# Optimization experiments

Measured on AMD Instinct MI355X. Metric: run time of the kernel, lower is better.

## Reference

```python
import jax, jax.numpy as jnp
import numpy as np

N, E, FIN, NH, FOUT = 50000, 800000, 128, 4, 16


def setup_inputs() -> dict:
    key = jax.random.key(0)
    ks = jax.random.split(key, 6)
    x = jax.random.normal(ks[0], (N, FIN), dtype=jnp.float32)
    edge_index = jax.random.randint(ks[1], (2, E), 0, N, dtype=jnp.int64)
    w_proj = jax.random.normal(ks[2], (NH * FOUT, FIN), dtype=jnp.float32) * 0.05
    a_src = jax.random.normal(ks[3], (NH, FOUT), dtype=jnp.float32) * 0.1
    a_trg = jax.random.normal(ks[4], (NH, FOUT), dtype=jnp.float32) * 0.1
    w_skip = jax.random.normal(ks[5], (NH * FOUT, FIN), dtype=jnp.float32) * 0.05
    return {"x": x, "edge_index": edge_index, "w_proj": w_proj,
            "a_src": a_src, "a_trg": a_trg, "w_skip": w_skip}


def reference(x, edge_index, w_proj, a_src, a_trg, w_skip):
    # Dropout is identity in eval mode.
    src, trg = edge_index[0], edge_index[1]
    # Project: [N, NH, FOUT]
    proj = (x @ w_proj.T).reshape(N, NH, FOUT)
    # Per-node attention logits: [N, NH]
    s_src = jnp.einsum('nhf,hf->nh', proj, a_src)
    s_trg = jnp.einsum('nhf,hf->nh', proj, a_trg)
    # Lift to edges and score: [E, NH]
    scores = jax.nn.leaky_relu(s_src[src] + s_trg[trg], negative_slope=0.2)
    # Global-max-shifted exp (matches original, which subtracts the global max)
    exp_scores = jnp.exp(scores - jnp.max(scores))
    # Segment-wise softmax denominator over target nodes
    denom = jax.ops.segment_sum(exp_scores, trg, num_segments=N)  # [N, NH]
    attn = exp_scores / (denom[trg] + 1e-16)                      # [E, NH]
    # Weighted aggregation of lifted source features: [N, NH, FOUT]
    weighted = proj[src] * attn[:, :, None]
    agg = jax.ops.segment_sum(weighted, trg, num_segments=N)
    # Skip projection (FOUT != FIN branch) and concat over heads
    out = agg + (x @ w_skip.T).reshape(N, NH, FOUT)
    out = out.reshape(N, NH * FOUT)
    return jax.nn.elu(out)
```

## Files before the change

### kernel.cpp

```cpp
#include <hip/hip_runtime.h>
#include <cstddef>

#define N_NODES 50000
#define N_EDGES 800000
#define FIN     128
#define NH      4
#define FOUT    16
#define COUT    64
#define STRIPS  (N_NODES / 16)
#define PAIRS   ((STRIPS + 1) / 2)
#define SCAN_BLOCKS ((N_NODES + 255) / 256)
#define NB      128
#define CHUNK   (N_EDGES / NB)
#define HW4     (N_NODES / 4)
#define HBYTES  (HW4 * 4)
#define NQ      4
#define BPQ     (NB / NQ)
#define PBLK    ((HW4 + 255) / 256)
#define E4      (N_EDGES / 4)
#define E4B     ((E4 + 255) / 256)

typedef __bf16 bf16x8 __attribute__((ext_vector_type(8)));
typedef float  f32x4  __attribute__((ext_vector_type(4)));

__global__ __launch_bounds__(256) void k1_mfma(
    const float* __restrict__ x, const __bf16* __restrict__ wb,
    const float* __restrict__ asrc, const float* __restrict__ atrg,
    __bf16* __restrict__ projb, float* __restrict__ ssrc, float* __restrict__ strg,
    float* __restrict__ outv)
{
    const int lane = threadIdx.x & 63;
    const int wid  = blockIdx.x * 4 + (threadIdx.x >> 6);
    const int pair = wid >> 1;
    const int half = wid & 1;
    if (pair >= PAIRS) return;
    const int r = lane & 15;
    const int g = lane >> 4;
    const int row0 = pair * 32;

    bf16x8 bfr[4][4];
    #pragma unroll
    for (int j = 0; j < 4; ++j) {
        const __bf16* wrow = wb + (size_t)(half * 64 + j * 16 + r) * FIN;
        #pragma unroll
        for (int kk = 0; kk < 4; ++kk)
            bfr[j][kk] = *reinterpret_cast<const bf16x8*>(wrow + kk * 32 + g * 8);
    }

    const int rowA0 = row0 + r;
    int rowA1 = row0 + 16 + r;
    if (rowA1 >= N_NODES) rowA1 = N_NODES - 1;
    const float* xr0 = x + (size_t)rowA0 * FIN + g * 8;
    const float* xr1 = x + (size_t)rowA1 * FIN + g * 8;
    bf16x8 af0[4], af1[4];
    #pragma unroll
    for (int kk = 0; kk < 4; ++kk) {
        float4 u0 = *reinterpret_cast<const float4*>(xr0 + kk * 32);
        float4 u1 = *reinterpret_cast<const float4*>(xr0 + kk * 32 + 4);
        float4 v0 = *reinterpret_cast<const float4*>(xr1 + kk * 32);
        float4 v1 = *reinterpret_cast<const float4*>(xr1 + kk * 32 + 4);
        bf16x8 a, b;
        a[0] = (__bf16)u0.x; a[1] = (__bf16)u0.y;
        a[2] = (__bf16)u0.z; a[3] = (__bf16)u0.w;
        a[4] = (__bf16)u1.x; a[5] = (__bf16)u1.y;
        a[6] = (__bf16)u1.z; a[7] = (__bf16)u1.w;
        b[0] = (__bf16)v0.x; b[1] = (__bf16)v0.y;
        b[2] = (__bf16)v0.z; b[3] = (__bf16)v0.w;
        b[4] = (__bf16)v1.x; b[5] = (__bf16)v1.y;
        b[6] = (__bf16)v1.z; b[7] = (__bf16)v1.w;
        af0[kk] = a; af1[kk] = b;
    }

    f32x4 acc0[4] = {{0.f,0.f,0.f,0.f},{0.f,0.f,0.f,0.f},
                     {0.f,0.f,0.f,0.f},{0.f,0.f,0.f,0.f}};
    f32x4 acc1[4] = {{0.f,0.f,0.f,0.f},{0.f,0.f,0.f,0.f},
                     {0.f,0.f,0.f,0.f},{0.f,0.f,0.f,0.f}};
    #pragma unroll
    for (int kk = 0; kk < 4; ++kk)
        #pragma unroll
        for (int j = 0; j < 4; ++j) {
            acc0[j] = __builtin_amdgcn_mfma_f32_16x16x32_bf16(
                          af0[kk], bfr[j][kk], acc0[j], 0, 0, 0);
            acc1[j] = __builtin_amdgcn_mfma_f32_16x16x32_bf16(
                          af1[kk], bfr[j][kk], acc1[j], 0, 0, 0);
        }

    if (!half) {
        #pragma unroll
        for (int j = 0; j < 4; ++j)
            #pragma unroll
            for (int q = 0; q < 4; ++q) {
                int n0 = row0 + g * 4 + q;
                int n1 = n0 + 16;
                projb[(size_t)n0 * COUT + j * 16 + r] = (__bf16)acc0[j][q];
                if (n1 < N_NODES)
                    projb[(size_t)n1 * COUT + j * 16 + r] = (__bf16)acc1[j][q];
            }
        #pragma unroll
        for (int j = 0; j < 4; ++j) {
            const float as = asrc[j * 16 + r];
            const float at = atrg[j * 16 + r];
            #pragma unroll
            for (int q = 0; q < 4; ++q) {
                float ts0 = acc0[j][q] * as, tt0 = acc0[j][q] * at;
                float ts1 = acc1[j][q] * as, tt1 = acc1[j][q] * at;
                ts0 += __shfl_xor(ts0, 1); ts0 += __shfl_xor(ts0, 2);
                ts0 += __shfl_xor(ts0, 4); ts0 += __shfl_xor(ts0, 8);
                tt0 += __shfl_xor(tt0, 1); tt0 += __shfl_xor(tt0, 2);
                tt0 += __shfl_xor(tt0, 4); tt0 += __shfl_xor(tt0, 8);
                ts1 += __shfl_xor(ts1, 1); ts1 += __shfl_xor(ts1, 2);
                ts1 += __shfl_xor(ts1, 4); ts1 += __shfl_xor(ts1, 8);
                tt1 += __shfl_xor(tt1, 1); tt1 += __shfl_xor(tt1, 2);
                tt1 += __shfl_xor(tt1, 4); tt1 += __shfl_xor(tt1, 8);
                if (r == 0) {
                    int n0 = row0 + g * 4 + q;
                    int n1 = n0 + 16;
                    ssrc[(size_t)n0 * NH + j] = ts0;
                    strg[(size_t)n0 * NH + j] = tt0;
                    if (n1 < N_NODES) {
                        ssrc[(size_t)n1 * NH + j] = ts1;
                        strg[(size_t)n1 * NH + j] = tt1;
                    }
                }
            }
        }
    } else {
        #pragma unroll
        for (int j = 0; j < 4; ++j)
            #pragma unroll
            for (int q = 0; q < 4; ++q) {
                int n0 = row0 + g * 4 + q;
                int n1 = n0 + 16;
                outv[(size_t)n0 * COUT + j * 16 + r] = acc0[j][q];
                if (n1 < N_NODES)
                    outv[(size_t)n1 * COUT + j * 16 + r] = acc1[j][q];
            }
    }
}

__global__ __launch_bounds__(1024) void k_hist(
    const int* __restrict__ ei, unsigned* __restrict__ histG,
    unsigned char* __restrict__ rank,
    const float* __restrict__ wproj, const float* __restrict__ wskip,
    __bf16* __restrict__ wb, int* __restrict__ scounter)
{
    if (blockIdx.x == NB) {
        const int tid = threadIdx.x;
        if (tid == 0) *scounter = 0;
        for (int gid = tid; gid < (128 * FIN) / 4; gid += 1024) {
            int row = gid >> 5;
            float4 v = (row < 64)
                ? reinterpret_cast<const float4*>(wproj)[gid]
                : reinterpret_cast<const float4*>(wskip)[gid - 2048];
            __bf16* o = wb + (size_t)gid * 4;
            o[0] = (__bf16)v.x; o[1] = (__bf16)v.y;
            o[2] = (__bf16)v.z; o[3] = (__bf16)v.w;
        }
        return;
    }
    extern __shared__ unsigned h[];
    const int t = threadIdx.x;
    for (int i = t; i < HW4; i += 1024) h[i] = 0;
    __syncthreads();
    const int base = blockIdx.x * CHUNK;
    for (int i = t; i < CHUNK; i += 1024) {
        int tg = ei[N_EDGES + base + i];
        int sh = (tg & 3) * 8;
        unsigned old = atomicAdd(&h[tg >> 2], 1u << sh);
        rank[base + i] = (unsigned char)((old >> sh) & 0xffu);
    }
    __syncthreads();
    unsigned* out = histG + (size_t)blockIdx.x * HW4;
    for (int i = t; i < HW4; i += 1024) out[i] = h[i];
}

__global__ __launch_bounds__(256) void k_colscanA(
    const unsigned* __restrict__ histG, unsigned* __restrict__ offG,
    unsigned* __restrict__ partial)
{
    int p = blockIdx.x * 256 + threadIdx.x;
    if (p >= HW4) return;
    int q = blockIdx.y;
    unsigned run = 0;
    #pragma unroll 4
    for (int b = q * BPQ; b < (q + 1) * BPQ; ++b) {
        unsigned v = histG[(size_t)b * HW4 + p];
        offG[(size_t)b * HW4 + p] = run;
        run += v;
    }
    partial[(size_t)q * HW4 + p] = run;
}

__global__ __launch_bounds__(256) void k_scanfuse(
    const unsigned* __restrict__ partial, unsigned* __restrict__ baseQ,
    int* __restrict__ deg, int* __restrict__ tmpExc,
    int* __restrict__ bsum, int* __restrict__ bOff,
    int* __restrict__ scounter)
{
    __shared__ int sm[256];
    __shared__ int isLast;
    const int t = threadIdx.x;
    if (t < 64) {
        int p = blockIdx.x * 64 + t;
        if (p < HW4) {
            unsigned s = 0;
            #pragma unroll
            for (int q = 0; q < NQ; ++q) {
                baseQ[(size_t)q * HW4 + p] = s;
                s += partial[(size_t)q * HW4 + p];
            }
            int4 d4 = make_int4((int)(s & 0xffu), (int)((s >> 8) & 0xffu),
                                (int)((s >> 16) & 0xffu), (int)(s >> 24));
            reinterpret_cast<int4*>(deg)[p] = d4;
            sm[4 * t + 0] = d4.x; sm[4 * t + 1] = d4.y;
            sm[4 * t + 2] = d4.z; sm[4 * t + 3] = d4.w;
        } else {
            sm[4 * t + 0] = 0; sm[4 * t + 1] = 0;
            sm[4 * t + 2] = 0; sm[4 * t + 3] = 0;
        }
    }
    __syncthreads();
    int v = sm[t];
    #pragma unroll
    for (int off = 1; off < 256; off <<= 1) {
        int x = (t >= off) ? sm[t - off] : 0;
        __syncthreads();
        sm[t] += x;
        __syncthreads();
    }
    int i = blockIdx.x * 256 + t;
    if (i < N_NODES) tmpExc[i] = sm[t] - v;
    if (t == 255) atomicExch(&bsum[blockIdx.x], sm[t]);
    __syncthreads();
    if (t == 0) {
        __threadfence();
        int old = atomicAdd(scounter, 1);
        isLast = (old == SCAN_BLOCKS - 1) ? 1 : 0;
    }
    __syncthreads();
    if (isLast) {
        int bv = (t < SCAN_BLOCKS) ? atomicAdd(&bsum[t], 0) : 0;
        sm[t] = bv;
        __syncthreads();
        #pragma unroll
        for (int off = 1; off < 256; off <<= 1) {
            int x = (t >= off) ? sm[t - off] : 0;
            __syncthreads();
            sm[t] += x;
            __syncthreads();
        }
        if (t < SCAN_BLOCKS) bOff[t] = sm[t] - bv;
    }
}

__global__ __launch_bounds__(256) void k_scatter(
    const int* __restrict__ ei, const unsigned char* __restrict__ rank,
    const unsigned* __restrict__ offG, const unsigned* __restrict__ baseQ,
    const int* __restrict__ tmpExc, const int* __restrict__ bOff,
    int* __restrict__ srcs)
{
    int e4 = blockIdx.x * 256 + threadIdx.x;
    if (e4 >= E4) return;
    int4 s4 = reinterpret_cast<const int4*>(ei)[e4];
    int4 t4 = reinterpret_cast<const int4*>(ei + N_EDGES)[e4];
    uchar4 r4 = reinterpret_cast<const uchar4*>(rank)[e4];
    const int e0 = e4 * 4;
    int ss[4] = {s4.x, s4.y, s4.z, s4.w};
    int tt[4] = {t4.x, t4.y, t4.z, t4.w};
    int rr[4] = {r4.x, r4.y, r4.z, r4.w};
    #pragma unroll
    for (int u = 0; u < 4; ++u) {
        int tg = tt[u];
        int b  = (e0 + u) / CHUNK;
        int sh = (tg & 3) * 8;
        unsigned cw = offG[(size_t)b * HW4 + (tg >> 2)]
                    + baseQ[(size_t)(b / BPQ) * HW4 + (tg >> 2)];
        int cross = (int)((cw >> sh) & 0xffu);
        int slot  = tmpExc[tg] + bOff[tg >> 8] + cross + rr[u];
        srcs[slot] = ss[u];
    }
}

__global__ __launch_bounds__(256) void k3_gather(
    const int* __restrict__ tmpExc, const int* __restrict__ bOff,
    const int* __restrict__ deg, const int* __restrict__ srcs,
    const float* __restrict__ ssrc, const float* __restrict__ strg,
    const __bf16* __restrict__ projb, float* __restrict__ outv)
{
    const int lane = threadIdx.x & 63;
    const int node = __builtin_amdgcn_readfirstlane(blockIdx.x * 4 + (threadIdx.x >> 6));
    if (node >= N_NODES) return;
    const int h = lane >> 4;
    const int begin = tmpExc[node] + bOff[node >> 8];
    const int dg    = deg[node];
    const float st  = strg[(size_t)node * NH + h];
    const float skip = outv[(size_t)node * COUT + lane];

    float acc = 0.f, dsum = 0.f;
    int i = 0;
    for (; i + 8 <= dg; i += 8) {
        int s[8]; float a[8], p[8];
        #pragma unroll
        for (int u = 0; u < 8; ++u) s[u] = srcs[begin + i + u];
        #pragma unroll
        for (int u = 0; u < 8; ++u) a[u] = ssrc[(size_t)s[u] * NH + h];
        #pragma unroll
        for (int u = 0; u < 8; ++u) p[u] = (float)projb[(size_t)s[u] * COUT + lane];
        #pragma unroll
        for (int u = 0; u < 8; ++u) {
            float z = a[u] + st;
            z = (z >= 0.f) ? z : 0.2f * z;
            float ez = __expf(z);
            dsum += ez;
            acc += ez * p[u];
        }
    }
    for (; i + 4 <= dg; i += 4) {
        int s[4]; float a[4], p[4];
        #pragma unroll
        for (int u = 0; u < 4; ++u) s[u] = srcs[begin + i + u];
        #pragma unroll
        for (int u = 0; u < 4; ++u) a[u] = ssrc[(size_t)s[u] * NH + h];
        #pragma unroll
        for (int u = 0; u < 4; ++u) p[u] = (float)projb[(size_t)s[u] * COUT + lane];
        #pragma unroll
        for (int u = 0; u < 4; ++u) {
            float z = a[u] + st;
            z = (z >= 0.f) ? z : 0.2f * z;
            float ez = __expf(z);
            dsum += ez;
            acc += ez * p[u];
        }
    }
    for (; i < dg; ++i) {
        int s = srcs[begin + i];
        float z = ssrc[(size_t)s * NH + h] + st;
        z = (z >= 0.f) ? z : 0.2f * z;
        float ez = __expf(z);
        float p  = (float)projb[(size_t)s * COUT + lane];
        dsum += ez;
        acc += ez * p;
    }
    float o = acc / (dsum + 1e-16f) + skip;
    o = (o > 0.f) ? o : expm1f(o);
    outv[(size_t)node * COUT + lane] = o;
}

extern "C" void kernel_launch(void* const* d_in, const int* in_sizes, int n_in,
                              void* d_out, int out_size, void* d_ws, size_t ws_size,
                              hipStream_t stream)
{
    const float* x     = (const float*)d_in[0];
    const int*   ei    = (const int*)  d_in[1];
    const float* wproj = (const float*)d_in[2];
    const float* asrc  = (const float*)d_in[3];
    const float* atrg  = (const float*)d_in[4];
    const float* wskip = (const float*)d_in[5];
    float* outv = (float*)d_out;

    __bf16* projb = (__bf16*)d_ws;
    float* base  = (float*)d_ws;
    float* ssrc  = base + (size_t)N_NODES * COUT;
    float* strg  = ssrc + (size_t)N_NODES * NH;
    int* deg     = (int*)(strg + (size_t)N_NODES * NH);
    int* tmpExc  = deg    + N_NODES;
    int* bsum    = tmpExc + N_NODES;
    int* bOff    = bsum   + 256;
    int* srcs    = bOff   + 256;
    unsigned* histG   = (unsigned*)(srcs + N_EDGES);
    unsigned* offG    = histG + (size_t)NB * HW4;
    unsigned* partial = offG  + (size_t)NB * HW4;
    unsigned* baseQ   = partial + (size_t)NQ * HW4;
    unsigned char* rank = (unsigned char*)(baseQ + (size_t)NQ * HW4);
    __bf16* wb   = (__bf16*)(rank + N_EDGES);
    int* scounter = (int*)(wb + 128 * FIN);

    k_hist<<<NB + 1, 1024, HBYTES, stream>>>(ei, histG, rank,
                                             wproj, wskip, wb, scounter);

    int k1_blocks = (PAIRS * 2 + 3) / 4;
    k1_mfma<<<k1_blocks, 256, 0, stream>>>(x, wb, asrc, atrg,
                                           projb, ssrc, strg, outv);

    k_colscanA<<<dim3(PBLK, NQ), 256, 0, stream>>>(histG, offG, partial);

    k_scanfuse<<<SCAN_BLOCKS, 256, 0, stream>>>(partial, baseQ, deg,
                                                tmpExc, bsum, bOff, scounter);

    k_scatter<<<E4B, 256, 0, stream>>>(ei, rank, offG, baseQ,
                                       tmpExc, bOff, srcs);

    int k3_blocks = (N_NODES + 3) / 4;
    k3_gather<<<k3_blocks, 256, 0, stream>>>(tmpExc, bOff, deg, srcs,
                                             ssrc, strg, projb, outv);
}
```

Baseline: 95.02 us.

## Split histogram blocks by node range and fuse column scan into CSR scan

The histogram kernel now runs two blocks per edge chunk, each covering half of the packed node range, which halves shared memory per block so more blocks can be resident. Each block still reads every target in its chunk and discards those outside its half. The two-pass column scan and scan-fuse kernels are merged into one kernel in which four threads per packed word scan the quarters and combine them through shared memory, removing one launch and the partial buffer. The cost is that edge reads in the histogram are doubled.

```diff
diff --git a/kernel.cpp b/kernel.cpp
--- a/kernel.cpp
+++ b/kernel.cpp
@@ -13,10 +13,10 @@
 #define NB      128
 #define CHUNK   (N_EDGES / NB)
 #define HW4     (N_NODES / 4)
-#define HBYTES  (HW4 * 4)
+#define HALFW   (HW4 / 2)
+#define HBYTES2 (HALFW * 4)
 #define NQ      4
 #define BPQ     (NB / NQ)
-#define PBLK    ((HW4 + 255) / 256)
 #define E4      (N_EDGES / 4)
 #define E4B     ((E4 + 255) / 256)
 
@@ -144,7 +144,7 @@
     const float* __restrict__ wproj, const float* __restrict__ wskip,
     __bf16* __restrict__ wb, int* __restrict__ scounter)
 {
-    if (blockIdx.x == NB) {
+    if (blockIdx.x == NB * 2) {
         const int tid = threadIdx.x;
         if (tid == 0) *scounter = 0;
         for (int gid = tid; gid < (128 * FIN) / 4; gid += 1024) {
@@ -159,66 +159,67 @@
         return;
     }
     extern __shared__ unsigned h[];
+    const int chunk = blockIdx.x >> 1;
+    const int vhalf = blockIdx.x & 1;
     const int t = threadIdx.x;
-    for (int i = t; i < HW4; i += 1024) h[i] = 0;
-    __syncthreads();
-    const int base = blockIdx.x * CHUNK;
+    for (int i = t; i < HALFW; i += 1024) h[i] = 0;
+    __syncthreads();
+    const int base = chunk * CHUNK;
+    const int plo  = vhalf * HALFW;
     for (int i = t; i < CHUNK; i += 1024) {
         int tg = ei[N_EDGES + base + i];
-        int sh = (tg & 3) * 8;
-        unsigned old = atomicAdd(&h[tg >> 2], 1u << sh);
-        rank[base + i] = (unsigned char)((old >> sh) & 0xffu);
-    }
-    __syncthreads();
-    unsigned* out = histG + (size_t)blockIdx.x * HW4;
-    for (int i = t; i < HW4; i += 1024) out[i] = h[i];
-}
-
-__global__ __launch_bounds__(256) void k_colscanA(
+        int p  = (tg >> 2) - plo;
+        if ((unsigned)p < (unsigned)HALFW) {
+            int sh = (tg & 3) * 8;
+            unsigned old = atomicAdd(&h[p], 1u << sh);
+            rank[base + i] = (unsigned char)((old >> sh) & 0xffu);
+        }
+    }
+    __syncthreads();
+    unsigned* out = histG + (size_t)chunk * HW4 + plo;
+    for (int i = t; i < HALFW; i += 1024) out[i] = h[i];
+}
+
+__global__ __launch_bounds__(256) void k_csr_scan(
     const unsigned* __restrict__ histG, unsigned* __restrict__ offG,
-    unsigned* __restrict__ partial)
-{
-    int p = blockIdx.x * 256 + threadIdx.x;
-    if (p >= HW4) return;
-    int q = blockIdx.y;
-    unsigned run = 0;
-    #pragma unroll 4
-    for (int b = q * BPQ; b < (q + 1) * BPQ; ++b) {
-        unsigned v = histG[(size_t)b * HW4 + p];
-        offG[(size_t)b * HW4 + p] = run;
-        run += v;
-    }
-    partial[(size_t)q * HW4 + p] = run;
-}
-
-__global__ __launch_bounds__(256) void k_scanfuse(
-    const unsigned* __restrict__ partial, unsigned* __restrict__ baseQ,
+    unsigned* __restrict__ baseQ,
     int* __restrict__ deg, int* __restrict__ tmpExc,
     int* __restrict__ bsum, int* __restrict__ bOff,
     int* __restrict__ scounter)
 {
+    __shared__ unsigned part[64][NQ];
     __shared__ int sm[256];
     __shared__ int isLast;
-    const int t = threadIdx.x;
-    if (t < 64) {
-        int p = blockIdx.x * 64 + t;
-        if (p < HW4) {
-            unsigned s = 0;
-            #pragma unroll
-            for (int q = 0; q < NQ; ++q) {
-                baseQ[(size_t)q * HW4 + p] = s;
-                s += partial[(size_t)q * HW4 + p];
-            }
-            int4 d4 = make_int4((int)(s & 0xffu), (int)((s >> 8) & 0xffu),
-                                (int)((s >> 16) & 0xffu), (int)(s >> 24));
-            reinterpret_cast<int4*>(deg)[p] = d4;
-            sm[4 * t + 0] = d4.x; sm[4 * t + 1] = d4.y;
-            sm[4 * t + 2] = d4.z; sm[4 * t + 3] = d4.w;
-        } else {
-            sm[4 * t + 0] = 0; sm[4 * t + 1] = 0;
-            sm[4 * t + 2] = 0; sm[4 * t + 3] = 0;
-        }
-    }
+    const int t  = threadIdx.x;
+    const int pl = t >> 2;
+    const int q  = t & 3;
+    const int p  = blockIdx.x * 64 + pl;
+    const bool valid = (p < HW4);
+
+    unsigned run = 0;
+    if (valid) {
+        #pragma unroll 4
+        for (int b = q * BPQ; b < (q + 1) * BPQ; ++b) {
+            unsigned v = histG[(size_t)b * HW4 + p];
+            offG[(size_t)b * HW4 + p] = run;
+            run += v;
+        }
+    }
+    part[pl][q] = run;
+    __syncthreads();
+
+    unsigned p0 = part[pl][0], p1 = part[pl][1],
+             p2 = part[pl][2], p3 = part[pl][3];
+    unsigned pre = (q > 0 ? p0 : 0u) + (q > 1 ? p1 : 0u) + (q > 2 ? p2 : 0u);
+    unsigned total = p0 + p1 + p2 + p3;
+    if (valid) {
+        baseQ[(size_t)q * HW4 + p] = pre;
+        if (q == 0)
+            reinterpret_cast<int4*>(deg)[p] =
+                make_int4((int)(total & 0xffu), (int)((total >> 8) & 0xffu),
+                          (int)((total >> 16) & 0xffu), (int)(total >> 24));
+    }
+    sm[t] = valid ? (int)((total >> (q * 8)) & 0xffu) : 0;
     __syncthreads();
     int v = sm[t];
     #pragma unroll
@@ -369,22 +370,19 @@
     int* srcs    = bOff   + 256;
     unsigned* histG   = (unsigned*)(srcs + N_EDGES);
     unsigned* offG    = histG + (size_t)NB * HW4;
-    unsigned* partial = offG  + (size_t)NB * HW4;
-    unsigned* baseQ   = partial + (size_t)NQ * HW4;
+    unsigned* baseQ   = offG  + (size_t)NB * HW4;
     unsigned char* rank = (unsigned char*)(baseQ + (size_t)NQ * HW4);
     __bf16* wb   = (__bf16*)(rank + N_EDGES);
     int* scounter = (int*)(wb + 128 * FIN);
 
-    k_hist<<<NB + 1, 1024, HBYTES, stream>>>(ei, histG, rank,
-                                             wproj, wskip, wb, scounter);
+    k_hist<<<NB * 2 + 1, 1024, HBYTES2, stream>>>(ei, histG, rank,
+                                                  wproj, wskip, wb, scounter);
 
     int k1_blocks = (PAIRS * 2 + 3) / 4;
     k1_mfma<<<k1_blocks, 256, 0, stream>>>(x, wb, asrc, atrg,
                                            projb, ssrc, strg, outv);
 
-    k_colscanA<<<dim3(PBLK, NQ), 256, 0, stream>>>(histG, offG, partial);
-
-    k_scanfuse<<<SCAN_BLOCKS, 256, 0, stream>>>(partial, baseQ, deg,
+    k_csr_scan<<<SCAN_BLOCKS, 256, 0, stream>>>(histG, offG, baseQ, deg,
                                                 tmpExc, bsum, bOff, scounter);
 
     k_scatter<<<E4B, 256, 0, stream>>>(ei, rank, offG, baseQ,
```

After: 94.11 us. No clear change (-1.0%).
